# Kernel tuning notes

Measured on AMD Instinct MI355X. Metric: run time of the kernel, lower is better.

The kernel has to match this reference:

```python
import jax, jax.numpy as jnp
import numpy as np

A = 128   # image height (x_shape[0])
B = 128   # image width  (x_shape[1]); must equal A for the matmuls to type-check
N = 64    # glimpse size
H_DIM = 512
BATCH = 2048


def _filterbanks(params):
    """Vectorized Gaussian filterbank construction (replaces the per-column loop).
    params: (5,) = [gt_X, gt_Y, log_var, log_dt, log_gamma].
    gt_X, gt_Y, d are detached in the original via fix_param() -> stop_gradient here.
    """
    gt_X = jax.lax.stop_gradient(params[0])
    gt_Y = jax.lax.stop_gradient(params[1])
    var = jnp.exp(params[2] + 1e-8)
    d = jax.lax.stop_gradient(jnp.exp(params[3]) * (max(A, B) - 1) / (N - 1))
    g_X = (A + 1) * (gt_X + 1) / 2
    g_Y = (B + 1) * (gt_Y + 1) / 2
    # torch.linspace(g + (-N/2-0.5)*d, g + (N-1-N/2-0.5)*d, N) == g + (i - N/2 - 0.5)*d
    offs = (jnp.arange(N, dtype=jnp.float32) - N / 2 - 0.5) * d
    mu_X = g_X + offs  # (N,)
    mu_Y = g_Y + offs  # (N,)
    a = jnp.arange(A, dtype=jnp.float32)
    b = jnp.arange(B, dtype=jnp.float32)
    F_X = jnp.exp(-(a[None, :] - mu_X[:, None]) ** 2 / (2 * var))  # (N, A)
    F_Y = jnp.exp(-(b[None, :] - mu_Y[:, None]) ** 2 / (2 * var))  # (N, B)
    # NOTE: original normalizes by the GLOBAL sum, not per-row.
    F_X = F_X / jnp.sum(F_X)
    F_Y = F_Y / jnp.sum(F_Y)
    return F_X, F_Y


def setup_inputs() -> dict:
    key = jax.random.key(0)
    k1, k2, k3, k4 = jax.random.split(key, 4)
    x = jax.random.normal(k1, (BATCH, A * B), dtype=jnp.float32)
    x_hat = jax.random.normal(k2, (BATCH, A * B), dtype=jnp.float32)
    h = jax.random.normal(k3, (BATCH, H_DIM), dtype=jnp.float32)
    # W_read: Linear(h_dim, 5). Small init so exp(log_var), exp(log_dt), exp(log_gamma) stay sane.
    W_read_w = jax.random.normal(k4, (5, H_DIM), dtype=jnp.float32) * 0.01
    W_read_b = jnp.zeros((5,), dtype=jnp.float32)
    return {"x": x, "x_hat": x_hat, "h": h, "W_read_w": W_read_w, "W_read_b": W_read_b}


def reference(x, x_hat, h, W_read_w, W_read_b):
    # params = W_read(h)[0]  -> uses only the first batch element's params (as in original)
    params = h[0] @ W_read_w.T + W_read_b  # (5,)
    gamma = jnp.exp(params[4])
    F_X, F_Y = _filterbanks(params)  # (N, A), (N, B)

    xr = x.reshape(-1, A, B)
    xh = x_hat.reshape(-1, A, B)
    # gamma * F_Y @ x @ F_X.T : (batch, N, N)
    x_filt = gamma * jnp.einsum('na,bac,mc->bnm', F_Y, xr, F_X)
    x_hat_filt = gamma * jnp.einsum('na,bac,mc->bnm', F_Y, xh, F_X)
    return jnp.concatenate([x_filt.reshape(-1, N * N), x_hat_filt.reshape(-1, N * N)], axis=1)
```

## Files before the change

kernel.cpp:

```cpp
#include <hip/hip_runtime.h>
#include <math.h>

#define A_DIM 128
#define N_G   64
#define HD    512

typedef short short8 __attribute__((ext_vector_type(8)));
typedef float floatx4 __attribute__((ext_vector_type(4)));

static __device__ __forceinline__ unsigned short f2bf(float f) {
  union { float f; unsigned u; } v; v.f = f;
  unsigned r = (v.u + 0x7fffu + ((v.u >> 16) & 1u)) >> 16;
  return (unsigned short)r;
}

static __device__ __forceinline__ short8 pack8(float4 a, float4 b) {
  short8 r;
  r[0] = (short)f2bf(a.x); r[1] = (short)f2bf(a.y);
  r[2] = (short)f2bf(a.z); r[3] = (short)f2bf(a.w);
  r[4] = (short)f2bf(b.x); r[5] = (short)f2bf(b.y);
  r[6] = (short)f2bf(b.z); r[7] = (short)f2bf(b.w);
  return r;
}

__global__ __launch_bounds__(512) void fb_setup_kernel(
    const float* __restrict__ h, const float* __restrict__ Ww,
    const float* __restrict__ Wb, unsigned short* __restrict__ FXfrag,
    unsigned short* __restrict__ FYfrag) {
  __shared__ float p[5];
  __shared__ float redX[8], redY[8];
  __shared__ float invs[2];
  const int tid = threadIdx.x, wave = tid >> 6, lane = tid & 63;

  if (wave < 5) {
    float s = 0.f;
    for (int k = lane; k < HD; k += 64) s += h[k] * Ww[wave * HD + k];
#pragma unroll
    for (int off = 32; off > 0; off >>= 1) s += __shfl_down(s, off);
    if (lane == 0) p[wave] = s + Wb[wave];
  }
  __syncthreads();

  const float gX = 64.5f * (p[0] + 1.0f);
  const float gY = 64.5f * (p[1] + 1.0f);
  const float var = expf(p[2] + 1e-8f);
  const float dd = expf(p[3]) * (127.0f / 63.0f);
  const float gamma = expf(p[4]);
  const float two_var = 2.0f * var;

  float sX = 0.f, sY = 0.f;
  for (int i = tid; i < N_G * A_DIM; i += 512) {
    const int n = i >> 7, a = i & 127;
    const float off_n = ((float)n - 32.5f) * dd;
    const float tx = (float)a - (gX + off_n);
    const float ty = (float)a - (gY + off_n);
    sX += expf(-(tx * tx) / two_var);
    sY += expf(-(ty * ty) / two_var);
  }
#pragma unroll
  for (int off = 32; off > 0; off >>= 1) {
    sX += __shfl_down(sX, off);
    sY += __shfl_down(sY, off);
  }
  if (lane == 0) { redX[wave] = sX; redY[wave] = sY; }
  __syncthreads();
  if (tid == 0) {
    float tX = 0.f, tY = 0.f;
#pragma unroll
    for (int w = 0; w < 8; ++w) { tX += redX[w]; tY += redY[w]; }
    invs[0] = 1.0f / tX;
    invs[1] = gamma / tY;
  }
  __syncthreads();
  const float isX = invs[0], isYg = invs[1];

  for (int i = tid; i < 4 * 4 * 64 * 8; i += 512) {
    const int j = i & 7;
    const int ln = (i >> 3) & 63;
    const int kk = (i >> 9) & 3;
    const int tl = (i >> 11) & 3;
    const int mn = tl * 16 + (ln & 15);
    const int ca = kk * 32 + ((ln >> 4) << 3) + j;
    const float off_mn = ((float)mn - 32.5f) * dd;
    const float tx = (float)ca - (gX + off_mn);
    const float ty = (float)ca - (gY + off_mn);
    FXfrag[i] = f2bf(expf(-(tx * tx) / two_var) * isX);
    FYfrag[i] = f2bf(expf(-(ty * ty) / two_var) * isYg);
  }
}

__global__ __launch_bounds__(256, 4) void glimpse_kernel(
    const float* __restrict__ x, const float* __restrict__ xh,
    const unsigned short* __restrict__ FXfrag,
    const unsigned short* __restrict__ FYfrag,
    float* __restrict__ out) {
  const int img = blockIdx.x;
  const int b = img >> 1, t = img & 1;
  const float* __restrict__ src = (t ? xh : x) + (size_t)b * (A_DIM * A_DIM);
  float* __restrict__ dst = out + (size_t)b * (2 * N_G * N_G) + t * (N_G * N_G);

  __shared__ __align__(16) unsigned short us[N_G * A_DIM];

  const int tid = threadIdx.x;
  const int w = tid >> 6, lane = tid & 63;
  const int quad = lane >> 4, lm = lane & 15;

  short8 aFy[4];

  {
    const float4* __restrict__ src4 = (const float4*)src;

    float4 u0[2][4], u1[2][4];
#pragma unroll
    for (int i = 0; i < 2; ++i)
#pragma unroll
      for (int kk = 0; kk < 4; ++kk) {
        const int idx = ((2 * w + i) * 16 + lm) * 32 + kk * 8 + quad * 2;
        u0[i][kk] = src4[idx];
        u1[i][kk] = src4[idx + 1];
      }

#pragma unroll
    for (int kk = 0; kk < 4; ++kk)
      aFy[kk] = *(const short8*)(FYfrag + ((size_t)(w * 4 + kk) * 64 + lane) * 8);

    short8 aF[2][4];
#pragma unroll
    for (int i = 0; i < 2; ++i)
#pragma unroll
      for (int kk = 0; kk < 4; ++kk)
        aF[i][kk] = pack8(u0[i][kk], u1[i][kk]);

    floatx4 acc[2][4];
#pragma unroll
    for (int i = 0; i < 2; ++i)
#pragma unroll
      for (int j = 0; j < 4; ++j) acc[i][j] = (floatx4)0.f;

#pragma unroll
    for (int kk = 0; kk < 4; ++kk) {
      short8 bF[4];
#pragma unroll
      for (int j = 0; j < 4; ++j)
        bF[j] = *(const short8*)(FXfrag + ((size_t)(j * 4 + kk) * 64 + lane) * 8);
#pragma unroll
      for (int i = 0; i < 2; ++i)
#pragma unroll
        for (int j = 0; j < 4; ++j)
          acc[i][j] = __builtin_amdgcn_mfma_f32_16x16x32_bf16(aF[i][kk], bF[j], acc[i][j], 0, 0, 0);
    }

#pragma unroll
    for (int i = 0; i < 2; ++i) {
      const int ch = (2 * w + i) * 2 + (quad >> 1);
      const int half = (quad & 1) * 4;
#pragma unroll
      for (int j = 0; j < 4; ++j) {
        uint2 pk;
        pk.x = (unsigned)f2bf(acc[i][j][0]) | ((unsigned)f2bf(acc[i][j][1]) << 16);
        pk.y = (unsigned)f2bf(acc[i][j][2]) | ((unsigned)f2bf(acc[i][j][3]) << 16);
        *(uint2*)&us[(j * 16 + lm) * A_DIM + ((ch ^ lm) << 3) + half] = pk;
      }
    }
  }
  __syncthreads();

  {
    floatx4 acc2[4];
#pragma unroll
    for (int j = 0; j < 4; ++j) acc2[j] = (floatx4)0.f;

#pragma unroll
    for (int kk = 0; kk < 4; ++kk) {
#pragma unroll
      for (int mt = 0; mt < 4; ++mt) {
        const int ch = (kk * 4 + quad) ^ lm;
        const short8 bF = *(const short8*)&us[(mt * 16 + lm) * A_DIM + (ch << 3)];
        acc2[mt] = __builtin_amdgcn_mfma_f32_16x16x32_bf16(aFy[kk], bF, acc2[mt], 0, 0, 0);
      }
    }

#pragma unroll
    for (int mt = 0; mt < 4; ++mt)
#pragma unroll
      for (int r = 0; r < 4; ++r)
        dst[(w * 16 + quad * 4 + r) * N_G + mt * 16 + lm] = acc2[mt][r];
  }
}

extern "C" void kernel_launch(void* const* d_in, const int* in_sizes, int n_in,
                              void* d_out, int out_size, void* d_ws, size_t ws_size,
                              hipStream_t stream) {
  const float* x  = (const float*)d_in[0];
  const float* xh = (const float*)d_in[1];
  const float* h  = (const float*)d_in[2];
  const float* Ww = (const float*)d_in[3];
  const float* Wb = (const float*)d_in[4];
  float* out = (float*)d_out;

  unsigned short* FXfrag = (unsigned short*)d_ws;
  unsigned short* FYfrag = FXfrag + 4 * 4 * 64 * 8;

  fb_setup_kernel<<<1, 512, 0, stream>>>(h, Ww, Wb, FXfrag, FYfrag);
  glimpse_kernel<<<4096, 256, 0, stream>>>(x, xh, FXfrag, FYfrag, out);
}
```

Measured before the change: 313.9 us.

## Fuse filterbank setup into glimpse kernel and process both images per block

Removes the separate single-block setup kernel by recomputing the params, normalisation sums and filterbank fragments inside every glimpse block. FX goes to LDS and FY stays in registers. Each block now handles both x and x_hat for one batch element, prefetching the second image's loads while the first image is computed. This trades redundant per-block exp work and lower occupancy for one less launch and better latency overlap.

```diff
diff --git a/kernel.cpp b/kernel.cpp
--- a/kernel.cpp
+++ b/kernel.cpp
@@ -23,33 +23,62 @@
   return r;
 }
 
-__global__ __launch_bounds__(512) void fb_setup_kernel(
+__global__ __launch_bounds__(256, 2) void glimpse_kernel(
+    const float* __restrict__ x, const float* __restrict__ xh,
     const float* __restrict__ h, const float* __restrict__ Ww,
-    const float* __restrict__ Wb, unsigned short* __restrict__ FXfrag,
-    unsigned short* __restrict__ FYfrag) {
-  __shared__ float p[5];
-  __shared__ float redX[8], redY[8];
-  __shared__ float invs[2];
-  const int tid = threadIdx.x, wave = tid >> 6, lane = tid & 63;
-
-  if (wave < 5) {
+    const float* __restrict__ Wb, float* __restrict__ out) {
+  __shared__ __align__(16) unsigned short us[2][N_G * A_DIM];
+  __shared__ __align__(16) unsigned short fxt[4 * 4 * 64 * 8];
+  __shared__ float p_lds[5];
+  __shared__ float red[8];
+
+  const int b = blockIdx.x;
+  const float* __restrict__ src0 = x + (size_t)b * (A_DIM * A_DIM);
+  const float* __restrict__ src1 = xh + (size_t)b * (A_DIM * A_DIM);
+  float* __restrict__ dst0 = out + (size_t)b * (2 * N_G * N_G);
+
+  const int tid = threadIdx.x;
+  const int w = tid >> 6, lane = tid & 63;
+  const int quad = lane >> 4, lm = lane & 15;
+
+  float4 u0[2][4], u1[2][4];
+  {
+    const float4* __restrict__ s4 = (const float4*)src0;
+#pragma unroll
+    for (int i = 0; i < 2; ++i)
+#pragma unroll
+      for (int kk = 0; kk < 4; ++kk) {
+        const int idx = ((2 * w + i) * 16 + lm) * 32 + kk * 8 + quad * 2;
+        u0[i][kk] = s4[idx];
+        u1[i][kk] = s4[idx + 1];
+      }
+  }
+
+  {
     float s = 0.f;
-    for (int k = lane; k < HD; k += 64) s += h[k] * Ww[wave * HD + k];
+    for (int k = lane; k < HD; k += 64) s += h[k] * Ww[w * HD + k];
 #pragma unroll
     for (int off = 32; off > 0; off >>= 1) s += __shfl_down(s, off);
-    if (lane == 0) p[wave] = s + Wb[wave];
-  }
-  __syncthreads();
-
-  const float gX = 64.5f * (p[0] + 1.0f);
-  const float gY = 64.5f * (p[1] + 1.0f);
-  const float var = expf(p[2] + 1e-8f);
-  const float dd = expf(p[3]) * (127.0f / 63.0f);
-  const float gamma = expf(p[4]);
+    if (lane == 0) p_lds[w] = s + Wb[w];
+    if (w == 0) {
+      float s4v = 0.f;
+      for (int k = lane; k < HD; k += 64) s4v += h[k] * Ww[4 * HD + k];
+#pragma unroll
+      for (int off = 32; off > 0; off >>= 1) s4v += __shfl_down(s4v, off);
+      if (lane == 0) p_lds[4] = s4v + Wb[4];
+    }
+  }
+  __syncthreads();
+
+  const float gX = 64.5f * (p_lds[0] + 1.0f);
+  const float gY = 64.5f * (p_lds[1] + 1.0f);
+  const float var = expf(p_lds[2] + 1e-8f);
+  const float dd = expf(p_lds[3]) * (127.0f / 63.0f);
+  const float gamma = expf(p_lds[4]);
   const float two_var = 2.0f * var;
 
   float sX = 0.f, sY = 0.f;
-  for (int i = tid; i < N_G * A_DIM; i += 512) {
+  for (int i = tid; i < N_G * A_DIM; i += 256) {
     const int n = i >> 7, a = i & 127;
     const float off_n = ((float)n - 32.5f) * dd;
     const float tx = (float)a - (gX + off_n);
@@ -62,75 +91,70 @@
     sX += __shfl_down(sX, off);
     sY += __shfl_down(sY, off);
   }
-  if (lane == 0) { redX[wave] = sX; redY[wave] = sY; }
-  __syncthreads();
-  if (tid == 0) {
-    float tX = 0.f, tY = 0.f;
-#pragma unroll
-    for (int w = 0; w < 8; ++w) { tX += redX[w]; tY += redY[w]; }
-    invs[0] = 1.0f / tX;
-    invs[1] = gamma / tY;
-  }
-  __syncthreads();
-  const float isX = invs[0], isYg = invs[1];
-
-  for (int i = tid; i < 4 * 4 * 64 * 8; i += 512) {
-    const int j = i & 7;
-    const int ln = (i >> 3) & 63;
-    const int kk = (i >> 9) & 3;
-    const int tl = (i >> 11) & 3;
-    const int mn = tl * 16 + (ln & 15);
-    const int ca = kk * 32 + ((ln >> 4) << 3) + j;
-    const float off_mn = ((float)mn - 32.5f) * dd;
-    const float tx = (float)ca - (gX + off_mn);
-    const float ty = (float)ca - (gY + off_mn);
-    FXfrag[i] = f2bf(expf(-(tx * tx) / two_var) * isX);
-    FYfrag[i] = f2bf(expf(-(ty * ty) / two_var) * isYg);
-  }
-}
-
-__global__ __launch_bounds__(256, 4) void glimpse_kernel(
-    const float* __restrict__ x, const float* __restrict__ xh,
-    const unsigned short* __restrict__ FXfrag,
-    const unsigned short* __restrict__ FYfrag,
-    float* __restrict__ out) {
-  const int img = blockIdx.x;
-  const int b = img >> 1, t = img & 1;
-  const float* __restrict__ src = (t ? xh : x) + (size_t)b * (A_DIM * A_DIM);
-  float* __restrict__ dst = out + (size_t)b * (2 * N_G * N_G) + t * (N_G * N_G);
-
-  __shared__ __align__(16) unsigned short us[N_G * A_DIM];
-
-  const int tid = threadIdx.x;
-  const int w = tid >> 6, lane = tid & 63;
-  const int quad = lane >> 4, lm = lane & 15;
+  if (lane == 0) { red[w * 2] = sX; red[w * 2 + 1] = sY; }
+  __syncthreads();
+  float tX = 0.f, tY = 0.f;
+#pragma unroll
+  for (int wv = 0; wv < 4; ++wv) { tX += red[wv * 2]; tY += red[wv * 2 + 1]; }
+  const float isX = 1.0f / tX;
+  const float isYg = gamma / tY;
+
+#pragma unroll
+  for (int c = 0; c < 4; ++c) {
+    const int ibase = c * 2048 + tid * 8;
+    short8 v;
+#pragma unroll
+    for (int j = 0; j < 8; ++j) {
+      const int i = ibase + j;
+      const int jj = i & 7;
+      const int ln = (i >> 3) & 63;
+      const int kk = (i >> 9) & 3;
+      const int tl = (i >> 11) & 3;
+      const int mn = tl * 16 + (ln & 15);
+      const int ca = kk * 32 + ((ln >> 4) << 3) + jj;
+      const float off_mn = ((float)mn - 32.5f) * dd;
+      const float tx = (float)ca - (gX + off_mn);
+      v[j] = (short)f2bf(expf(-(tx * tx) / two_var) * isX);
+    }
+    *(short8*)&fxt[ibase] = v;
+  }
 
   short8 aFy[4];
-
-  {
-    const float4* __restrict__ src4 = (const float4*)src;
-
-    float4 u0[2][4], u1[2][4];
+#pragma unroll
+  for (int kk = 0; kk < 4; ++kk) {
+    short8 v;
+#pragma unroll
+    for (int j = 0; j < 8; ++j) {
+      const int mn = w * 16 + lm;
+      const int ca = kk * 32 + quad * 8 + j;
+      const float off_mn = ((float)mn - 32.5f) * dd;
+      const float ty = (float)ca - (gY + off_mn);
+      v[j] = (short)f2bf(expf(-(ty * ty) / two_var) * isYg);
+    }
+    aFy[kk] = v;
+  }
+  __syncthreads();
+
+  short8 aF[2][4];
+#pragma unroll
+  for (int i = 0; i < 2; ++i)
+#pragma unroll
+    for (int kk = 0; kk < 4; ++kk)
+      aF[i][kk] = pack8(u0[i][kk], u1[i][kk]);
+
+  {
+    const float4* __restrict__ s4 = (const float4*)src1;
 #pragma unroll
     for (int i = 0; i < 2; ++i)
 #pragma unroll
       for (int kk = 0; kk < 4; ++kk) {
         const int idx = ((2 * w + i) * 16 + lm) * 32 + kk * 8 + quad * 2;
-        u0[i][kk] = src4[idx];
-        u1[i][kk] = src4[idx + 1];
-      }
-
-#pragma unroll
-    for (int kk = 0; kk < 4; ++kk)
-      aFy[kk] = *(const short8*)(FYfrag + ((size_t)(w * 4 + kk) * 64 + lane) * 8);
-
-    short8 aF[2][4];
-#pragma unroll
-    for (int i = 0; i < 2; ++i)
-#pragma unroll
-      for (int kk = 0; kk < 4; ++kk)
-        aF[i][kk] = pack8(u0[i][kk], u1[i][kk]);
-
+        u0[i][kk] = s4[idx];
+        u1[i][kk] = s4[idx + 1];
+      }
+  }
+
+  {
     floatx4 acc[2][4];
 #pragma unroll
     for (int i = 0; i < 2; ++i)
@@ -142,7 +166,7 @@
       short8 bF[4];
 #pragma unroll
       for (int j = 0; j < 4; ++j)
-        bF[j] = *(const short8*)(FXfrag + ((size_t)(j * 4 + kk) * 64 + lane) * 8);
+        bF[j] = *(const short8*)&fxt[((j * 4 + kk) * 64 + lane) * 8];
 #pragma unroll
       for (int i = 0; i < 2; ++i)
 #pragma unroll
@@ -159,7 +183,7 @@
         uint2 pk;
         pk.x = (unsigned)f2bf(acc[i][j][0]) | ((unsigned)f2bf(acc[i][j][1]) << 16);
         pk.y = (unsigned)f2bf(acc[i][j][2]) | ((unsigned)f2bf(acc[i][j][3]) << 16);
-        *(uint2*)&us[(j * 16 + lm) * A_DIM + ((ch ^ lm) << 3) + half] = pk;
+        *(uint2*)&us[0][(j * 16 + lm) * A_DIM + ((ch ^ lm) << 3) + half] = pk;
       }
     }
   }
@@ -169,22 +193,82 @@
     floatx4 acc2[4];
 #pragma unroll
     for (int j = 0; j < 4; ++j) acc2[j] = (floatx4)0.f;
-
 #pragma unroll
     for (int kk = 0; kk < 4; ++kk) {
 #pragma unroll
       for (int mt = 0; mt < 4; ++mt) {
         const int ch = (kk * 4 + quad) ^ lm;
-        const short8 bF = *(const short8*)&us[(mt * 16 + lm) * A_DIM + (ch << 3)];
-        acc2[mt] = __builtin_amdgcn_mfma_f32_16x16x32_bf16(aFy[kk], bF, acc2[mt], 0, 0, 0);
-      }
-    }
-
+        const short8 bF8 = *(const short8*)&us[0][(mt * 16 + lm) * A_DIM + (ch << 3)];
+        acc2[mt] = __builtin_amdgcn_mfma_f32_16x16x32_bf16(aFy[kk], bF8, acc2[mt], 0, 0, 0);
+      }
+    }
 #pragma unroll
     for (int mt = 0; mt < 4; ++mt)
 #pragma unroll
       for (int r = 0; r < 4; ++r)
-        dst[(w * 16 + quad * 4 + r) * N_G + mt * 16 + lm] = acc2[mt][r];
+        dst0[(w * 16 + quad * 4 + r) * N_G + mt * 16 + lm] = acc2[mt][r];
+  }
+
+#pragma unroll
+  for (int i = 0; i < 2; ++i)
+#pragma unroll
+    for (int kk = 0; kk < 4; ++kk)
+      aF[i][kk] = pack8(u0[i][kk], u1[i][kk]);
+
+  {
+    floatx4 acc[2][4];
+#pragma unroll
+    for (int i = 0; i < 2; ++i)
+#pragma unroll
+      for (int j = 0; j < 4; ++j) acc[i][j] = (floatx4)0.f;
+
+#pragma unroll
+    for (int kk = 0; kk < 4; ++kk) {
+      short8 bF[4];
+#pragma unroll
+      for (int j = 0; j < 4; ++j)
+        bF[j] = *(const short8*)&fxt[((j * 4 + kk) * 64 + lane) * 8];
+#pragma unroll
+      for (int i = 0; i < 2; ++i)
+#pragma unroll
+        for (int j = 0; j < 4; ++j)
+          acc[i][j] = __builtin_amdgcn_mfma_f32_16x16x32_bf16(aF[i][kk], bF[j], acc[i][j], 0, 0, 0);
+    }
+
+#pragma unroll
+    for (int i = 0; i < 2; ++i) {
+      const int ch = (2 * w + i) * 2 + (quad >> 1);
+      const int half = (quad & 1) * 4;
+#pragma unroll
+      for (int j = 0; j < 4; ++j) {
+        uint2 pk;
+        pk.x = (unsigned)f2bf(acc[i][j][0]) | ((unsigned)f2bf(acc[i][j][1]) << 16);
+        pk.y = (unsigned)f2bf(acc[i][j][2]) | ((unsigned)f2bf(acc[i][j][3]) << 16);
+        *(uint2*)&us[1][(j * 16 + lm) * A_DIM + ((ch ^ lm) << 3) + half] = pk;
+      }
+    }
+  }
+  __syncthreads();
+
+  {
+    floatx4 acc2[4];
+#pragma unroll
+    for (int j = 0; j < 4; ++j) acc2[j] = (floatx4)0.f;
+#pragma unroll
+    for (int kk = 0; kk < 4; ++kk) {
+#pragma unroll
+      for (int mt = 0; mt < 4; ++mt) {
+        const int ch = (kk * 4 + quad) ^ lm;
+        const short8 bF8 = *(const short8*)&us[1][(mt * 16 + lm) * A_DIM + (ch << 3)];
+        acc2[mt] = __builtin_amdgcn_mfma_f32_16x16x32_bf16(aFy[kk], bF8, acc2[mt], 0, 0, 0);
+      }
+    }
+    float* __restrict__ dst1 = dst0 + N_G * N_G;
+#pragma unroll
+    for (int mt = 0; mt < 4; ++mt)
+#pragma unroll
+      for (int r = 0; r < 4; ++r)
+        dst1[(w * 16 + quad * 4 + r) * N_G + mt * 16 + lm] = acc2[mt][r];
   }
 }
 
@@ -198,9 +282,5 @@
   const float* Wb = (const float*)d_in[4];
   float* out = (float*)d_out;
 
-  unsigned short* FXfrag = (unsigned short*)d_ws;
-  unsigned short* FYfrag = FXfrag + 4 * 4 * 64 * 8;
-
-  fb_setup_kernel<<<1, 512, 0, stream>>>(h, Ww, Wb, FXfrag, FYfrag);
-  glimpse_kernel<<<4096, 256, 0, stream>>>(x, xh, FXfrag, FYfrag, out);
-}
+  glimpse_kernel<<<2048, 256, 0, stream>>>(x, xh, h, Ww, Wb, out);
+}
```

New measurement: 336.9 us. 7.3% more time.
